# Performance work log

Hardware: AMD Instinct MI355X
Metric: run time of the kernel (lower is better)

## Reference

```python
import jax, jax.numpy as jnp
import numpy as np

D_MODEL = 1024
N_HEADS = 16
D_FF = 4 * D_MODEL
EPS = 1e-5


def _layer_norm(x, g, b):
    mu = jnp.mean(x, axis=-1, keepdims=True)
    var = jnp.mean(jnp.square(x - mu), axis=-1, keepdims=True)
    return (x - mu) * jax.lax.rsqrt(var + EPS) * g + b


def _mha(x, Wq, Wk, Wv, Wo, causal):
    B, S, D = x.shape
    H = N_HEADS
    Dh = D // H
    q = (x @ Wq).reshape(B, S, H, Dh)
    k = (x @ Wk).reshape(B, S, H, Dh)
    v = (x @ Wv).reshape(B, S, H, Dh)
    scores = jnp.einsum('bqhd,bkhd->bhqk', q, k) / jnp.sqrt(jnp.asarray(Dh, x.dtype))
    if causal:
        mask = jnp.tril(jnp.ones((S, S), dtype=bool))  # [S,S] causal mask
        scores = jnp.where(mask, scores, jnp.asarray(-1e9, x.dtype))
    attn = jax.nn.softmax(scores, axis=-1)
    out = jnp.einsum('bhqk,bkhd->bqhd', attn, v).reshape(B, S, D)
    return out @ Wo


def _ffn(x, W1, b1, W2, b2):
    return jax.nn.relu(x @ W1 + b1) @ W2 + b2


def setup_inputs() -> dict:
    key = jax.random.key(0)
    ks = jax.random.split(key, 12)
    sd = 1.0 / np.sqrt(D_MODEL)
    sf = 1.0 / np.sqrt(D_FF)
    B, S = 4, 1024
    return {
        'X': jax.random.normal(ks[0], (B, S, D_MODEL), jnp.float32),
        'Wq1': jax.random.normal(ks[1], (D_MODEL, D_MODEL), jnp.float32) * sd,
        'Wk1': jax.random.normal(ks[2], (D_MODEL, D_MODEL), jnp.float32) * sd,
        'Wv1': jax.random.normal(ks[3], (D_MODEL, D_MODEL), jnp.float32) * sd,
        'Wo1': jax.random.normal(ks[4], (D_MODEL, D_MODEL), jnp.float32) * sd,
        'Wq2': jax.random.normal(ks[5], (D_MODEL, D_MODEL), jnp.float32) * sd,
        'Wk2': jax.random.normal(ks[6], (D_MODEL, D_MODEL), jnp.float32) * sd,
        'Wv2': jax.random.normal(ks[7], (D_MODEL, D_MODEL), jnp.float32) * sd,
        'Wo2': jax.random.normal(ks[8], (D_MODEL, D_MODEL), jnp.float32) * sd,
        'ln_g': jnp.ones((D_MODEL,), jnp.float32),
        'ln_b': jnp.zeros((D_MODEL,), jnp.float32),
        'W1': jax.random.normal(ks[9], (D_MODEL, D_FF), jnp.float32) * sd,
        'b1': jnp.zeros((D_FF,), jnp.float32),
        'W2': jax.random.normal(ks[10], (D_FF, D_MODEL), jnp.float32) * sf,
        'b2': jnp.zeros((D_MODEL,), jnp.float32),
    }


def reference(X, Wq1, Wk1, Wv1, Wo1, Wq2, Wk2, Wv2, Wo2, ln_g, ln_b, W1, b1, W2, b2):
    # Faithful to the torch module (including its unusual residual wiring
    # and the single shared LayerNorm used at all three sites).
    masked = _mha(X, Wq1, Wk1, Wv1, Wo1, causal=True)
    norm_masked = X + _layer_norm(masked, ln_g, ln_b)
    attn2 = _mha(norm_masked, Wq2, Wk2, Wv2, Wo2, causal=False)
    norm_attn2 = attn2 + _layer_norm(attn2, ln_g, ln_b)
    ff = _ffn(norm_attn2, W1, b1, W2, b2)
    return norm_attn2 + _layer_norm(ff, ln_g, ln_b)
```

## Files before the change

### kernel.cpp

```cpp
#include <hip/hip_runtime.h>
#include <hip/hip_bf16.h>

#define D_MODEL 1024
#define N_HEADS 16
#define DH 64
#define D_FF   4096
#define SEQ    1024
#define BATCH  4
#define TOK    (BATCH*SEQ)
#define EPS    1e-5f
#define SCALE  0.125f
#define QSCL   0.18033688f

typedef unsigned short USHORT;
typedef __attribute__((ext_vector_type(8))) short short8v;
typedef __attribute__((ext_vector_type(4))) float f32x4;

__device__ __forceinline__ USHORT f2bf(float f) {
    unsigned int u; __builtin_memcpy(&u, &f, 4);
    u += 0x7fffu + ((u >> 16) & 1u);
    return (USHORT)(u >> 16);
}
__device__ __forceinline__ USHORT f2bf_fast(float f) {
    unsigned int u; __builtin_memcpy(&u, &f, 4);
    return (USHORT)((u + 0x8000u) >> 16);
}
__device__ __forceinline__ unsigned pk2bf(float lo, float hi) {
    __hip_bfloat162 h = __float22bfloat162_rn(make_float2(lo, hi));
    unsigned u; __builtin_memcpy(&u, &h, 4);
    return u;
}
__device__ __forceinline__ float bf2f(USHORT s) {
    unsigned int u = ((unsigned int)s) << 16;
    float f; __builtin_memcpy(&f, &u, 4);
    return f;
}
__device__ __forceinline__ float max3f(float a, float b, float c) {
    return fmaxf(fmaxf(a, b), c);
}

__device__ __forceinline__ short8v ld_frag(const USHORT* lds, int row, int c8) {
    return *reinterpret_cast<const short8v*>(
        &lds[row * 64 + (((c8) ^ (row & 7)) << 3)]);
}

#define GLDS(gsrc, ldst) \
    __builtin_amdgcn_global_load_lds( \
        (const __attribute__((address_space(1))) void*)(gsrc), \
        (__attribute__((address_space(3))) void*)(ldst), 16, 0, 0)

#define WAITVM(n) asm volatile("s_waitcnt vmcnt(" #n ")" ::: "memory")

__global__ __launch_bounds__(512) void gemm_k256_kernel(
    const USHORT* __restrict__ A, const USHORT* __restrict__ Bt,
    float* __restrict__ Cf, USHORT* __restrict__ Cb, USHORT* __restrict__ Ck,
    USHORT* __restrict__ VtOut,
    int M, int N, int K, const float* __restrict__ bias, int relu, int qkv)
{
    __shared__ USHORT As[2][256 * 64];
    __shared__ USHORT Bs[2][256 * 64];

    const int tid = threadIdx.x;
    const int l   = tid & 63;
    const int w   = tid >> 6;
    const int wr  = w >> 2, wc = w & 3;
    const int lr  = l & 15, lg = l >> 4;

    const int gx  = gridDim.x;
    const int nwg = gx * gridDim.y;
    const int lin = blockIdx.y * gx + blockIdx.x;
    const int swz = (lin & 7) * (nwg >> 3) + (lin >> 3);
    const int m0  = (swz / gx) * 256, n0 = (swz % gx) * 256;

    const USHORT* aS[4]; const USHORT* bS[4]; int dOf[4];
#pragma unroll
    for (int p = 0; p < 4; ++p) {
        const int q = p * 512 + tid;
        const int row = q >> 3, cu = q & 7;
        const int cs = ((cu ^ (row & 7)) << 3);
        aS[p] = A  + (size_t)(m0 + row) * K + cs;
        bS[p] = Bt + (size_t)(n0 + row) * K + cs;
        dOf[p] = (p * 512 + w * 64) * 8;
    }

    auto stage = [&](int buf, int k0) {
#pragma unroll
        for (int p = 0; p < 4; ++p) {
            GLDS(aS[p] + k0, &As[buf][dOf[p]]);
            GLDS(bS[p] + k0, &Bs[buf][dOf[p]]);
        }
    };

    f32x4 acc[8][4];
#pragma unroll
    for (int i = 0; i < 8; ++i)
#pragma unroll
        for (int j = 0; j < 4; ++j) acc[i][j] = (f32x4){0.f, 0.f, 0.f, 0.f};

    const int nk = K >> 6;
    stage(0, 0);

    for (int t = 0; t < nk; ++t) {
        const int cur = t & 1;
        if (t + 1 < nk) {
            stage(cur ^ 1, (t + 1) << 6);
            WAITVM(8);
        } else {
            WAITVM(0);
        }
        __builtin_amdgcn_s_barrier();

#pragma unroll
        for (int ks = 0; ks < 2; ++ks) {
            short8v bfr[4];
#pragma unroll
            for (int ni = 0; ni < 4; ++ni)
                bfr[ni] = ld_frag(Bs[cur], wc * 64 + ni * 16 + lr, ks * 4 + lg);
            __builtin_amdgcn_s_setprio(1);
#pragma unroll
            for (int mi = 0; mi < 8; ++mi) {
                short8v af = ld_frag(As[cur], wr * 128 + mi * 16 + lr, ks * 4 + lg);
#pragma unroll
                for (int ni = 0; ni < 4; ++ni)
                    acc[mi][ni] = __builtin_amdgcn_mfma_f32_16x16x32_bf16(
                        af, bfr[ni], acc[mi][ni], 0, 0, 0);
            }
            __builtin_amdgcn_s_setprio(0);
        }
        __builtin_amdgcn_s_barrier();
    }

    if (qkv) {
#pragma unroll
        for (int mi = 0; mi < 8; ++mi) {
            const int row = m0 + wr * 128 + mi * 16 + (l >> 4) * 4;
#pragma unroll
            for (int ni = 0; ni < 4; ++ni) {
                const int col = n0 + wc * 64 + ni * 16 + lr;
                if (col < 2048) {
                    USHORT* dst = (col < 1024) ? Cb : Ck;
                    const float scl = (col < 1024) ? QSCL : 1.f;
                    const int c = col & 1023;
#pragma unroll
                    for (int j = 0; j < 4; ++j)
                        dst[(size_t)(row + j) * D_MODEL + c] =
                            f2bf(acc[mi][ni][j] * scl);
                } else {
                    const int c = col - 2048;
                    const int bb = row >> 10, jr = row & 1023;
                    const int hh = c >> 6, dd = c & 63;
                    uint2 pk = make_uint2(
                        pk2bf(acc[mi][ni][0], acc[mi][ni][1]),
                        pk2bf(acc[mi][ni][2], acc[mi][ni][3]));
                    *reinterpret_cast<uint2*>(
                        &VtOut[((size_t)(bb * 16 + hh) * 64 + dd) * 1024 + jr]) = pk;
                }
            }
        }
    } else {
#pragma unroll
        for (int mi = 0; mi < 8; ++mi) {
            const int row = m0 + wr * 128 + mi * 16 + (l >> 4) * 4;
#pragma unroll
            for (int ni = 0; ni < 4; ++ni) {
                const int col = n0 + wc * 64 + ni * 16 + lr;
                const float bv = bias ? bias[col] : 0.f;
#pragma unroll
                for (int j = 0; j < 4; ++j) {
                    float v = acc[mi][ni][j] + bv;
                    if (relu) v = fmaxf(v, 0.f);
                    const size_t idx = (size_t)(row + j) * N + col;
                    if (Cf) Cf[idx] = v;
                    if (Cb) Cb[idx] = f2bf(v);
                }
            }
        }
    }
}

__global__ __launch_bounds__(512) void gemm_k128c_kernel(
    const USHORT* __restrict__ A, const USHORT* __restrict__ Bt,
    USHORT* __restrict__ Pa, USHORT* __restrict__ Pb,
    int M, int N, int K)
{
    __shared__ USHORT As[2][128 * 64];
    __shared__ USHORT Bs[2][128 * 64];

    const int tid = threadIdx.x;
    const int l   = tid & 63;
    const int w   = tid >> 6;
    const int wr  = w >> 2, wc = w & 3;
    const int lr  = l & 15, lg = l >> 4;

    const int gx  = gridDim.x;
    const int nwg = gx * gridDim.y;
    const int lin = blockIdx.y * gx + blockIdx.x;
    const int swz = (lin & 7) * (nwg >> 3) + (lin >> 3);
    const int my  = swz / gx;
    const int mt  = M >> 7;
    const int part = my / mt;
    const int m0  = (my % mt) << 7;
    const int n0  = (swz % gx) * 128;
    const int koff = part * (K >> 1);
    USHORT* dst = part ? Pb : Pa;

    const USHORT* aS[2]; const USHORT* bS[2]; int dOf[2];
#pragma unroll
    for (int p = 0; p < 2; ++p) {
        const int q = p * 512 + tid;
        const int row = q >> 3, cu = q & 7;
        const int cs = ((cu ^ (row & 7)) << 3);
        aS[p] = A  + (size_t)(m0 + row) * K + cs;
        bS[p] = Bt + (size_t)(n0 + row) * K + cs;
        dOf[p] = (p * 512 + w * 64) * 8;
    }

    auto stage = [&](int buf, int k0) {
#pragma unroll
        for (int p = 0; p < 2; ++p) {
            GLDS(aS[p] + k0, &As[buf][dOf[p]]);
            GLDS(bS[p] + k0, &Bs[buf][dOf[p]]);
        }
    };

    f32x4 acc[4][2];
#pragma unroll
    for (int i = 0; i < 4; ++i)
#pragma unroll
        for (int j = 0; j < 2; ++j) acc[i][j] = (f32x4){0.f, 0.f, 0.f, 0.f};

    const int nk = K >> 7;
    stage(0, koff);

    for (int t = 0; t < nk; ++t) {
        const int cur = t & 1;
        if (t + 1 < nk) {
            stage(cur ^ 1, koff + ((t + 1) << 6));
            WAITVM(4);
        } else {
            WAITVM(0);
        }
        __builtin_amdgcn_s_barrier();

#pragma unroll
        for (int ks = 0; ks < 2; ++ks) {
            short8v bfr[2];
#pragma unroll
            for (int ni = 0; ni < 2; ++ni)
                bfr[ni] = ld_frag(Bs[cur], wc * 32 + ni * 16 + lr, ks * 4 + lg);
            __builtin_amdgcn_s_setprio(1);
#pragma unroll
            for (int mi = 0; mi < 4; ++mi) {
                short8v af = ld_frag(As[cur], wr * 64 + mi * 16 + lr, ks * 4 + lg);
#pragma unroll
                for (int ni = 0; ni < 2; ++ni)
                    acc[mi][ni] = __builtin_amdgcn_mfma_f32_16x16x32_bf16(
                        af, bfr[ni], acc[mi][ni], 0, 0, 0);
            }
            __builtin_amdgcn_s_setprio(0);
        }
        __builtin_amdgcn_s_barrier();
    }

#pragma unroll
    for (int mi = 0; mi < 4; ++mi) {
        const int row = m0 + wr * 64 + mi * 16 + (l >> 4) * 4;
#pragma unroll
        for (int ni = 0; ni < 2; ++ni) {
            const int col = n0 + wc * 32 + ni * 16 + lr;
#pragma unroll
            for (int j = 0; j < 4; ++j)
                dst[(size_t)(row + j) * N + col] = f2bf(acc[mi][ni][j]);
        }
    }
}

struct TcvtB4 {
    const float* s0; const float* s1; const float* s2; const float* s3;
    USHORT* d0; USHORT* d1; USHORT* d2; USHORT* d3;
};

__device__ __forceinline__ void tcvt_body(
    const float* __restrict__ W, USHORT* __restrict__ Wt, int K, int N)
{
    __shared__ USHORT L[64][65];
    const int tid = threadIdx.x;
    const int tx = tid & 15, ty = tid >> 4;
    const int n0 = blockIdx.x * 64, k0 = blockIdx.y * 64;
#pragma unroll
    for (int r = 0; r < 4; ++r) {
        int kr = ty + 16 * r;
        float4 v = *reinterpret_cast<const float4*>(
            &W[(size_t)(k0 + kr) * N + n0 + tx * 4]);
        L[tx * 4 + 0][kr] = f2bf(v.x);
        L[tx * 4 + 1][kr] = f2bf(v.y);
        L[tx * 4 + 2][kr] = f2bf(v.z);
        L[tx * 4 + 3][kr] = f2bf(v.w);
    }
    __syncthreads();
#pragma unroll
    for (int r = 0; r < 4; ++r) {
        int nr = ty + 16 * r;
        ushort4 o = make_ushort4(L[nr][tx * 4 + 0], L[nr][tx * 4 + 1],
                                 L[nr][tx * 4 + 2], L[nr][tx * 4 + 3]);
        *reinterpret_cast<ushort4*>(&Wt[(size_t)(n0 + nr) * K + k0 + tx * 4]) = o;
    }
}

__global__ __launch_bounds__(256) void tcvt_kernel(
    const float* __restrict__ W, USHORT* __restrict__ Wt, int K, int N)
{
    tcvt_body(W, Wt, K, N);
}

__global__ __launch_bounds__(256) void tcvt4_kernel(TcvtB4 p, int K, int N)
{
    const int z = blockIdx.z;
    const float* W = (z == 0) ? p.s0 : (z == 1) ? p.s1 : (z == 2) ? p.s2 : p.s3;
    USHORT*    Wt = (z == 0) ? p.d0 : (z == 1) ? p.d1 : (z == 2) ? p.d2 : p.d3;
    tcvt_body(W, Wt, K, N);
}

__global__ __launch_bounds__(256) void f2b_kernel(
    const float* __restrict__ in, USHORT* __restrict__ out, int n4)
{
    int i = blockIdx.x * 256 + threadIdx.x;
    if (i < n4) {
        float4 v = reinterpret_cast<const float4*>(in)[i];
        reinterpret_cast<ushort4*>(out)[i] =
            make_ushort4(f2bf(v.x), f2bf(v.y), f2bf(v.z), f2bf(v.w));
    }
}

__global__ __launch_bounds__(256) void attn_mfma_kernel(
    const USHORT* __restrict__ Q, const USHORT* __restrict__ K,
    const USHORT* __restrict__ Vt, USHORT* __restrict__ O, int causal)
{
    __shared__ USHORT smem[24576];

    const int tid = threadIdx.x;
    const int l  = tid & 63;
    const int w  = tid >> 6;
    const int lr = l & 15;
    const int lg = l >> 4;

    const int lin = blockIdx.y * 8 + blockIdx.x;
    const int swz = (lin & 7) * 64 + (lin >> 3);
    const int qt = swz & 7;
    const int bh = swz >> 3;
    const int h = bh & 15, b = bh >> 4;
    const int q0 = qt * 128;

    const USHORT* gq  = Q  + (size_t)(b * SEQ + q0) * D_MODEL + h * DH;
    const USHORT* gk0 = K  + (size_t)b * SEQ * D_MODEL + h * DH;
    const USHORT* gv0 = Vt + (size_t)bh * DH * SEQ;

    auto stageK = [&](int buf, int kt) {
        USHORT* dst = smem + buf * 4096;
        const size_t base = (size_t)kt * 64 * 1024;
#pragma unroll
        for (int p = 0; p < 2; ++p) {
            const int q = p * 256 + tid;
            const int row = q >> 3, cu = q & 7;
            GLDS(gk0 + base + (size_t)row * 1024 + ((cu ^ (row & 7)) << 3),
                 dst + (p * 256 + w * 64) * 8);
        }
    };
    auto stageV = [&](int buf, int kt) {
        USHORT* dst = smem + 8192 + buf * 4096;
        const int j0 = kt * 64;
#pragma unroll
        for (int p = 0; p < 2; ++p) {
            const int q = p * 256 + tid;
            const int row = q >> 3, cu = q & 7;
            GLDS(gv0 + (size_t)row * 1024 + j0 + ((cu ^ (row & 7)) << 3),
                 dst + (p * 256 + w * 64) * 8);
        }
    };

#pragma unroll
    for (int p = 0; p < 4; ++p) {
        const int q = p * 256 + tid;
        const int row = q >> 3, cu = q & 7;
        GLDS(gq + (size_t)row * 1024 + ((cu ^ (row & 7)) << 3),
             smem + 16384 + (p * 256 + w * 64) * 8);
    }
    stageK(0, 0);
    stageV(0, 0);

    f32x4 oacc[2][4];
    float m_[2], l_[2];
#pragma unroll
    for (int s = 0; s < 2; ++s) {
        m_[s] = -1e30f; l_[s] = 0.f;
#pragma unroll
        for (int d = 0; d < 4; ++d) oacc[s][d] = (f32x4){0.f, 0.f, 0.f, 0.f};
    }

    int paddr[2][4];
#pragma unroll
    for (int s = 0; s < 2; ++s) {
        const int row = s * 16 + lr;
#pragma unroll
        for (int jb = 0; jb < 4; ++jb) {
            const int cu = jb * 2 + (lg >> 1);
            paddr[s][jb] = row * 64 + ((cu ^ (row & 7)) << 3) + (lg & 1) * 4;
        }
    }

    __syncthreads();
    short8v qa[2][2];
#pragma unroll
    for (int s = 0; s < 2; ++s) {
        qa[s][0] = ld_frag(smem + 16384, w * 32 + s * 16 + lr, lg);
        qa[s][1] = ld_frag(smem + 16384, w * 32 + s * 16 + lr, 4 + lg);
    }
    __syncthreads();
    USHORT* PsW = smem + 16384 + w * 2048;

    const int ntile = causal ? (qt * 2 + 2) : (SEQ / 64);
    for (int kt = 0; kt < ntile; ++kt) {
        const int cur = kt & 1;
        if (kt + 1 < ntile) {
            stageK(cur ^ 1, kt + 1);
            stageV(cur ^ 1, kt + 1);
        }
        const int j0 = kt * 64;
        const USHORT* KsC = smem + cur * 4096;
        const USHORT* VsC = smem + 8192 + cur * 4096;

        f32x4 sa[2][4];
        __builtin_amdgcn_s_setprio(1);
#pragma unroll
        for (int jb = 0; jb < 4; ++jb) {
            short8v kf0 = ld_frag(KsC, jb * 16 + lr, lg);
            short8v kf1 = ld_frag(KsC, jb * 16 + lr, 4 + lg);
#pragma unroll
            for (int s = 0; s < 2; ++s) {
                sa[s][jb] = (f32x4){0.f, 0.f, 0.f, 0.f};
                sa[s][jb] = __builtin_amdgcn_mfma_f32_16x16x32_bf16(
                    kf0, qa[s][0], sa[s][jb], 0, 0, 0);
                sa[s][jb] = __builtin_amdgcn_mfma_f32_16x16x32_bf16(
                    kf1, qa[s][1], sa[s][jb], 0, 0, 0);
            }
        }
        __builtin_amdgcn_s_setprio(0);

        if (causal && kt >= ntile - 2) {
#pragma unroll
            for (int s = 0; s < 2; ++s) {
                const int qrow = q0 + w * 32 + s * 16 + lr;
#pragma unroll
                for (int jb = 0; jb < 4; ++jb)
#pragma unroll
                    for (int r = 0; r < 4; ++r)
                        if ((j0 + jb * 16 + lg * 4 + r) > qrow)
                            sa[s][jb][r] = -1e30f;
            }
        }

        float tm[2];
#pragma unroll
        for (int s = 0; s < 2; ++s) {
            float t1 = max3f(sa[s][0][0], sa[s][0][1], sa[s][0][2]);
            float t2 = max3f(sa[s][0][3], sa[s][1][0], sa[s][1][1]);
            float t3 = max3f(sa[s][1][2], sa[s][1][3], sa[s][2][0]);
            float t4 = max3f(sa[s][2][1], sa[s][2][2], sa[s][2][3]);
            float t5 = max3f(sa[s][3][0], sa[s][3][1], sa[s][3][2]);
            float tv = fmaxf(max3f(max3f(t1, t2, t3), t4, t5), sa[s][3][3]);
            tv = fmaxf(tv, __shfl_xor(tv, 16));
            tv = fmaxf(tv, __shfl_xor(tv, 32));
            tm[s] = tv;
        }

        const bool anyf = (tm[0] > m_[0] + 8.f) | (tm[1] > m_[1] + 8.f);
        if (__ballot(anyf)) {
            float sc[2];
#pragma unroll
            for (int s = 0; s < 2; ++s) {
                const float mn = (tm[s] > m_[s] + 8.f) ? tm[s] : m_[s];
                sc[s] = exp2f(m_[s] - mn);
                l_[s] *= sc[s];
                m_[s] = mn;
            }
#pragma unroll
            for (int s = 0; s < 2; ++s)
#pragma unroll
                for (int r = 0; r < 4; ++r) {
                    const float scr = __shfl(sc[s], (l & 48) | (lg * 4 + r));
#pragma unroll
                    for (int d = 0; d < 4; ++d) oacc[s][d][r] *= scr;
                }
        }

#pragma unroll
        for (int s = 0; s < 2; ++s)
#pragma unroll
            for (int jb = 0; jb < 4; ++jb) {
                const float p0 = exp2f(sa[s][jb][0] - m_[s]);
                const float p1 = exp2f(sa[s][jb][1] - m_[s]);
                const float p2 = exp2f(sa[s][jb][2] - m_[s]);
                const float p3 = exp2f(sa[s][jb][3] - m_[s]);
                l_[s] += (p0 + p1) + (p2 + p3);
                *reinterpret_cast<uint2*>(&PsW[paddr[s][jb]]) =
                    make_uint2(pk2bf(p0, p1), pk2bf(p2, p3));
            }

        __builtin_amdgcn_s_setprio(1);
#pragma unroll
        for (int ks = 0; ks < 2; ++ks) {
            short8v pa[2];
#pragma unroll
            for (int s = 0; s < 2; ++s)
                pa[s] = ld_frag(PsW, s * 16 + lr, ks * 4 + lg);
#pragma unroll
            for (int d = 0; d < 4; ++d) {
                short8v vf = ld_frag(VsC, d * 16 + lr, ks * 4 + lg);
#pragma unroll
                for (int s = 0; s < 2; ++s)
                    oacc[s][d] = __builtin_amdgcn_mfma_f32_16x16x32_bf16(
                        pa[s], vf, oacc[s][d], 0, 0, 0);
            }
        }
        __builtin_amdgcn_s_setprio(0);
        __syncthreads();
    }

    USHORT* go = O + (size_t)(b * SEQ + q0 + w * 32) * D_MODEL + h * DH;
#pragma unroll
    for (int s = 0; s < 2; ++s) {
        float lv = l_[s];
        lv += __shfl_xor(lv, 16);
        lv += __shfl_xor(lv, 32);
        const float inv_own = 1.f / lv;
#pragma unroll
        for (int r = 0; r < 4; ++r) {
            const float inv = __shfl(inv_own, (l & 48) | (lg * 4 + r));
            const int qrow = s * 16 + lg * 4 + r;
#pragma unroll
            for (int d = 0; d < 4; ++d)
                go[(size_t)qrow * D_MODEL + d * 16 + lr] =
                    f2bf_fast(oacc[s][d][r] * inv);
        }
    }
}

__global__ __launch_bounds__(256) void ln_res_kernel(
    const USHORT* __restrict__ xb, const USHORT* __restrict__ xb2,
    const float* __restrict__ biasx,
    const float* __restrict__ resf, const USHORT* __restrict__ resb,
    const float* __restrict__ g, const float* __restrict__ bta,
    float* __restrict__ outf, USHORT* __restrict__ outb)
{
    __shared__ float red[256];
    __shared__ float s_mu, s_rstd;

    const int row = blockIdx.x;
    const int tid = threadIdx.x;
    ushort4 xv = reinterpret_cast<const ushort4*>(xb + (size_t)row * D_MODEL)[tid];
    float vx = bf2f(xv.x), vy = bf2f(xv.y), vz = bf2f(xv.z), vw = bf2f(xv.w);
    if (xb2) {
        ushort4 x2 = reinterpret_cast<const ushort4*>(
            xb2 + (size_t)row * D_MODEL)[tid];
        vx += bf2f(x2.x); vy += bf2f(x2.y); vz += bf2f(x2.z); vw += bf2f(x2.w);
    }
    if (biasx) {
        float4 bx = reinterpret_cast<const float4*>(biasx)[tid];
        vx += bx.x; vy += bx.y; vz += bx.z; vw += bx.w;
    }

    red[tid] = vx + vy + vz + vw;
    __syncthreads();
    for (int s = 128; s > 0; s >>= 1) {
        if (tid < s) red[tid] += red[tid + s];
        __syncthreads();
    }
    if (tid == 0) s_mu = red[0] * (1.f / D_MODEL);
    __syncthreads();
    const float mu = s_mu;

    float dx = vx - mu, dy = vy - mu, dz = vz - mu, dw = vw - mu;
    red[tid] = dx * dx + dy * dy + dz * dz + dw * dw;
    __syncthreads();
    for (int s = 128; s > 0; s >>= 1) {
        if (tid < s) red[tid] += red[tid + s];
        __syncthreads();
    }
    if (tid == 0) s_rstd = rsqrtf(red[0] * (1.f / D_MODEL) + EPS);
    __syncthreads();
    const float rstd = s_rstd;

    float4 rv;
    if (resf) {
        rv = reinterpret_cast<const float4*>(resf + (size_t)row * D_MODEL)[tid];
    } else if (resb) {
        ushort4 rb = reinterpret_cast<const ushort4*>(
            resb + (size_t)row * D_MODEL)[tid];
        rv = make_float4(bf2f(rb.x), bf2f(rb.y), bf2f(rb.z), bf2f(rb.w));
    } else {
        rv = make_float4(vx, vy, vz, vw);
    }
    float4 gv = reinterpret_cast<const float4*>(g)[tid];
    float4 bv = reinterpret_cast<const float4*>(bta)[tid];

    float4 o;
    o.x = rv.x + dx * rstd * gv.x + bv.x;
    o.y = rv.y + dy * rstd * gv.y + bv.y;
    o.z = rv.z + dz * rstd * gv.z + bv.z;
    o.w = rv.w + dw * rstd * gv.w + bv.w;
    reinterpret_cast<float4*>(outf + (size_t)row * D_MODEL)[tid] = o;
    if (outb)
        reinterpret_cast<ushort4*>(outb + (size_t)row * D_MODEL)[tid] =
            make_ushort4(f2bf(o.x), f2bf(o.y), f2bf(o.z), f2bf(o.w));
}

extern "C" void kernel_launch(void* const* d_in, const int* in_sizes, int n_in,
                              void* d_out, int out_size, void* d_ws, size_t ws_size,
                              hipStream_t stream)
{
    const float* X    = (const float*)d_in[0];
    const float* Wq1  = (const float*)d_in[1];
    const float* Wk1  = (const float*)d_in[2];
    const float* Wv1  = (const float*)d_in[3];
    const float* Wo1  = (const float*)d_in[4];
    const float* Wq2  = (const float*)d_in[5];
    const float* Wk2  = (const float*)d_in[6];
    const float* Wv2  = (const float*)d_in[7];
    const float* Wo2  = (const float*)d_in[8];
    const float* ln_g = (const float*)d_in[9];
    const float* ln_b = (const float*)d_in[10];
    const float* W1   = (const float*)d_in[11];
    const float* b1   = (const float*)d_in[12];
    const float* W2   = (const float*)d_in[13];
    const float* b2   = (const float*)d_in[14];

    const size_t MI = 1024 * 1024;
    USHORT* ws16 = (USHORT*)d_ws;
    USHORT* Wqkv1t = ws16;
    USHORT* scr0   = ws16;
    USHORT* Wo1t   = ws16 + 3 * MI;
    USHORT* Wqkv2t = ws16 + 4 * MI;
    USHORT* Wo2t   = ws16 + 7 * MI;
    USHORT* W2t    = ws16 + 8 * MI;
    USHORT* Xb     = ws16 + 12 * MI;
    USHORT* W1t    = Xb;
    USHORT* qb     = ws16 + 16 * MI;
    USHORT* kb     = ws16 + 20 * MI;
    USHORT* Vtb    = ws16 + 24 * MI;
    USHORT* t0b    = ws16 + 28 * MI;
    USHORT* hb     = qb;
    USHORT* t2b    = ws16 + 32 * MI;
    USHORT* t1b    = ws16 + 36 * MI;
    float*  t2     = (float*)(ws16 + 40 * MI);

    auto gemm256 = [&](const USHORT* A, const USHORT* Bt, float* Cf, USHORT* Cb,
                       int M, int N, int K, const float* bias, int relu) {
        gemm_k256_kernel<<<dim3(N / 256, M / 256), 512, 0, stream>>>(
            A, Bt, Cf, Cb, nullptr, nullptr, M, N, K, bias, relu, 0);
    };
    auto gemm_qkv = [&](const USHORT* A, const USHORT* Bt) {
        gemm_k256_kernel<<<dim3(3072 / 256, TOK / 256), 512, 0, stream>>>(
            A, Bt, nullptr, qb, kb, Vtb, TOK, 3072, D_MODEL, nullptr, 0, 1);
    };
    auto gemm128c = [&](const USHORT* A, const USHORT* Bt, USHORT* Pa, USHORT* Pb,
                        int M, int N, int K) {
        gemm_k128c_kernel<<<dim3(N / 128, (M / 128) * 2), 512, 0, stream>>>(
            A, Bt, Pa, Pb, M, N, K);
    };

    dim3 agrid(SEQ / 128, BATCH * N_HEADS);

    {
        TcvtB4 p1{Wq1, Wk1, Wv1, Wo1,
                  Wqkv1t, Wqkv1t + 1 * MI, Wqkv1t + 2 * MI, Wo1t};
        tcvt4_kernel<<<dim3(16, 16, 4), 256, 0, stream>>>(p1, D_MODEL, D_MODEL);
        TcvtB4 p2{Wq2, Wk2, Wv2, Wo2,
                  Wqkv2t, Wqkv2t + 1 * MI, Wqkv2t + 2 * MI, Wo2t};
        tcvt4_kernel<<<dim3(16, 16, 4), 256, 0, stream>>>(p2, D_MODEL, D_MODEL);
    }
    tcvt_kernel<<<dim3(D_MODEL / 64, D_FF / 64), 256, 0, stream>>>(
        W2, W2t, D_FF, D_MODEL);
    f2b_kernel<<<dim3(4096), 256, 0, stream>>>(X, Xb, TOK * D_MODEL / 4);

    gemm_qkv(Xb, Wqkv1t);
    attn_mfma_kernel<<<agrid, 256, 0, stream>>>(qb, kb, Vtb, t0b, 1);
    gemm128c(t0b, Wo1t, t2b, t1b, TOK, D_MODEL, D_MODEL);
    ln_res_kernel<<<dim3(TOK), 256, 0, stream>>>(t2b, t1b, nullptr, X, nullptr,
                                                 ln_g, ln_b, t2, t2b);
    tcvt_kernel<<<dim3(D_FF / 64, D_MODEL / 64), 256, 0, stream>>>(
        W1, W1t, D_MODEL, D_FF);

    gemm_qkv(t2b, Wqkv2t);
    attn_mfma_kernel<<<agrid, 256, 0, stream>>>(qb, kb, Vtb, t0b, 0);
    gemm128c(t0b, Wo2t, scr0, t1b, TOK, D_MODEL, D_MODEL);
    ln_res_kernel<<<dim3(TOK), 256, 0, stream>>>(scr0, t1b, nullptr,
                                                 nullptr, nullptr,
                                                 ln_g, ln_b, t2, t2b);

    gemm256(t2b, W1t, nullptr, hb, TOK, D_FF, D_MODEL, b1, 1);
    gemm128c(hb, W2t, t2b, t1b, TOK, D_MODEL, D_FF);
    ln_res_kernel<<<dim3(TOK), 256, 0, stream>>>(t2b, t1b, b2, t2, nullptr,
                                                 ln_g, ln_b, (float*)d_out, nullptr);
}
```

Before: 335.1 us.

## Interleave half-tile loads with MFMA phases in 256x256 GEMM; rebalance causal attention tiles

The 256x256 GEMM now splits each operand tile into halves and issues the next K-step's loads in four phases interleaved with MFMA groups. B is prefetched two steps ahead, and the trailing barrier per iteration is removed. This targets the load/compute serialization of the old whole-tile double buffer. The causal attention kernel also reverses the query-tile order for half of the head blocks so heavy and light causal tiles are mixed across workgroups. The extra barriers per K-step and the tighter buffer-reuse ordering add synchronization risk.

Result: faster. 311.3 us (-7.1%).

```diff
diff --git a/kernel.cpp b/kernel.cpp
--- a/kernel.cpp
+++ b/kernel.cpp
@@ -51,14 +51,13 @@
 
 #define WAITVM(n) asm volatile("s_waitcnt vmcnt(" #n ")" ::: "memory")
 
-__global__ __launch_bounds__(512) void gemm_k256_kernel(
+__global__ __launch_bounds__(512) void gemm_k256p8_kernel(
     const USHORT* __restrict__ A, const USHORT* __restrict__ Bt,
     float* __restrict__ Cf, USHORT* __restrict__ Cb, USHORT* __restrict__ Ck,
     USHORT* __restrict__ VtOut,
     int M, int N, int K, const float* __restrict__ bias, int relu, int qkv)
 {
-    __shared__ USHORT As[2][256 * 64];
-    __shared__ USHORT Bs[2][256 * 64];
+    __shared__ USHORT smem[65536];
 
     const int tid = threadIdx.x;
     const int l   = tid & 63;
@@ -72,23 +71,18 @@
     const int swz = (lin & 7) * (nwg >> 3) + (lin >> 3);
     const int m0  = (swz / gx) * 256, n0 = (swz % gx) * 256;
 
-    const USHORT* aS[4]; const USHORT* bS[4]; int dOf[4];
-#pragma unroll
-    for (int p = 0; p < 4; ++p) {
-        const int q = p * 512 + tid;
-        const int row = q >> 3, cu = q & 7;
-        const int cs = ((cu ^ (row & 7)) << 3);
-        aS[p] = A  + (size_t)(m0 + row) * K + cs;
-        bS[p] = Bt + (size_t)(n0 + row) * K + cs;
-        dOf[p] = (p * 512 + w * 64) * 8;
-    }
-
-    auto stage = [&](int buf, int k0) {
-#pragma unroll
-        for (int p = 0; p < 4; ++p) {
-            GLDS(aS[p] + k0, &As[buf][dOf[p]]);
-            GLDS(bS[p] + k0, &Bs[buf][dOf[p]]);
-        }
+    const int srow = tid >> 3;
+    const int scol = ((tid & 7) ^ (srow & 7)) << 3;
+    const USHORT* aS0 = A  + (size_t)(m0 + srow) * K + scol;
+    const USHORT* bS0 = Bt + (size_t)(n0 + srow) * K + scol;
+    const int dof0 = (w * 64) * 8;
+    const int dof1 = (512 + w * 64) * 8;
+
+    auto stageH = [&](int mat, int d, int h, int koff) {
+        const USHORT* src = (mat ? bS0 : aS0) + (size_t)(h * 128) * K + koff;
+        USHORT* dst = smem + mat * 32768 + d * 16384 + h * 8192;
+        GLDS(src, dst + dof0);
+        GLDS(src + (size_t)64 * K, dst + dof1);
     };
 
     f32x4 acc[8][4];
@@ -98,36 +92,56 @@
         for (int j = 0; j < 4; ++j) acc[i][j] = (f32x4){0.f, 0.f, 0.f, 0.f};
 
     const int nk = K >> 6;
-    stage(0, 0);
-
-    for (int t = 0; t < nk; ++t) {
-        const int cur = t & 1;
-        if (t + 1 < nk) {
-            stage(cur ^ 1, (t + 1) << 6);
-            WAITVM(8);
-        } else {
-            WAITVM(0);
-        }
-        __builtin_amdgcn_s_barrier();
-
-#pragma unroll
-        for (int ks = 0; ks < 2; ++ks) {
-            short8v bfr[4];
-#pragma unroll
-            for (int ni = 0; ni < 4; ++ni)
-                bfr[ni] = ld_frag(Bs[cur], wc * 64 + ni * 16 + lr, ks * 4 + lg);
+
+    stageH(0, 0, 0, 0);  stageH(0, 0, 1, 0);
+    stageH(1, 0, 0, 0);  stageH(1, 0, 1, 0);
+    stageH(1, 1, 0, 64); stageH(1, 1, 1, 64);
+
+    for (int kt = 0; kt < nk; ++kt) {
+        const int d = kt & 1;
+        const USHORT* Ah = smem + d * 16384 + wr * 8192;
+        const USHORT* Bh = smem + 32768 + d * 16384 + (wc >> 1) * 8192;
+        const int brow = (wc & 1) * 64;
+        short8v bfr[4][2];
+
+#pragma unroll
+        for (int g = 0; g < 4; ++g) {
+            if (g == 0) {
+                if (kt + 1 < nk) { WAITVM(4); } else { WAITVM(0); }
+            }
+            __builtin_amdgcn_s_barrier();
+
+            if (g == 0) {
+#pragma unroll
+                for (int ni = 0; ni < 4; ++ni) {
+                    bfr[ni][0] = ld_frag(Bh, brow + ni * 16 + lr, lg);
+                    bfr[ni][1] = ld_frag(Bh, brow + ni * 16 + lr, 4 + lg);
+                }
+            }
+            short8v a0k0 = ld_frag(Ah, (g * 2) * 16 + lr, lg);
+            short8v a0k1 = ld_frag(Ah, (g * 2) * 16 + lr, 4 + lg);
+            short8v a1k0 = ld_frag(Ah, (g * 2 + 1) * 16 + lr, lg);
+            short8v a1k1 = ld_frag(Ah, (g * 2 + 1) * 16 + lr, 4 + lg);
+
+            if (g == 0 && kt + 1 < nk) stageH(0, (kt + 1) & 1, 0, (kt + 1) * 64);
+            if (g == 1 && kt + 1 < nk) stageH(0, (kt + 1) & 1, 1, (kt + 1) * 64);
+            if (g == 2 && kt + 2 < nk) stageH(1, kt & 1, 0, (kt + 2) * 64);
+            if (g == 3 && kt + 2 < nk) stageH(1, kt & 1, 1, (kt + 2) * 64);
+
             __builtin_amdgcn_s_setprio(1);
 #pragma unroll
-            for (int mi = 0; mi < 8; ++mi) {
-                short8v af = ld_frag(As[cur], wr * 128 + mi * 16 + lr, ks * 4 + lg);
-#pragma unroll
-                for (int ni = 0; ni < 4; ++ni)
-                    acc[mi][ni] = __builtin_amdgcn_mfma_f32_16x16x32_bf16(
-                        af, bfr[ni], acc[mi][ni], 0, 0, 0);
+            for (int ni = 0; ni < 4; ++ni) {
+                acc[g * 2][ni] = __builtin_amdgcn_mfma_f32_16x16x32_bf16(
+                    a0k0, bfr[ni][0], acc[g * 2][ni], 0, 0, 0);
+                acc[g * 2][ni] = __builtin_amdgcn_mfma_f32_16x16x32_bf16(
+                    a0k1, bfr[ni][1], acc[g * 2][ni], 0, 0, 0);
+                acc[g * 2 + 1][ni] = __builtin_amdgcn_mfma_f32_16x16x32_bf16(
+                    a1k0, bfr[ni][0], acc[g * 2 + 1][ni], 0, 0, 0);
+                acc[g * 2 + 1][ni] = __builtin_amdgcn_mfma_f32_16x16x32_bf16(
+                    a1k1, bfr[ni][1], acc[g * 2 + 1][ni], 0, 0, 0);
             }
             __builtin_amdgcn_s_setprio(0);
         }
-        __builtin_amdgcn_s_barrier();
     }
 
     if (qkv) {
@@ -346,7 +360,8 @@
 
     const int lin = blockIdx.y * 8 + blockIdx.x;
     const int swz = (lin & 7) * 64 + (lin >> 3);
-    const int qt = swz & 7;
+    const int qtr = swz & 7;
+    const int qt  = causal ? (qtr ^ (((swz >> 5) & 1) ? 7 : 0)) : qtr;
     const int bh = swz >> 3;
     const int h = bh & 15, b = bh >> 4;
     const int q0 = qt * 128;
@@ -653,13 +668,13 @@
     USHORT* t1b    = ws16 + 36 * MI;
     float*  t2     = (float*)(ws16 + 40 * MI);
 
-    auto gemm256 = [&](const USHORT* A, const USHORT* Bt, float* Cf, USHORT* Cb,
+    auto gemmBig = [&](const USHORT* A, const USHORT* Bt, float* Cf, USHORT* Cb,
                        int M, int N, int K, const float* bias, int relu) {
-        gemm_k256_kernel<<<dim3(N / 256, M / 256), 512, 0, stream>>>(
+        gemm_k256p8_kernel<<<dim3(N / 256, M / 256), 512, 0, stream>>>(
             A, Bt, Cf, Cb, nullptr, nullptr, M, N, K, bias, relu, 0);
     };
     auto gemm_qkv = [&](const USHORT* A, const USHORT* Bt) {
-        gemm_k256_kernel<<<dim3(3072 / 256, TOK / 256), 512, 0, stream>>>(
+        gemm_k256p8_kernel<<<dim3(3072 / 256, TOK / 256), 512, 0, stream>>>(
             A, Bt, nullptr, qb, kb, Vtb, TOK, 3072, D_MODEL, nullptr, 0, 1);
     };
     auto gemm128c = [&](const USHORT* A, const USHORT* Bt, USHORT* Pa, USHORT* Pb,
@@ -697,7 +712,7 @@
                                                  nullptr, nullptr,
                                                  ln_g, ln_b, t2, t2b);
 
-    gemm256(t2b, W1t, nullptr, hb, TOK, D_FF, D_MODEL, b1, 1);
+    gemmBig(t2b, W1t, nullptr, hb, TOK, D_FF, D_MODEL, b1, 1);
     gemm128c(hb, W2t, t2b, t1b, TOK, D_MODEL, D_FF);
     ln_res_kernel<<<dim3(TOK), 256, 0, stream>>>(t2b, t1b, b2, t2, nullptr,
                                                  ln_g, ln_b, (float*)d_out, nullptr);
```
